# Kernel tuning notes

Hardware: AMD Instinct MI355X
Metric: run time of the kernel (lower is better)

The kernel has to match this reference:

```python
import jax, jax.numpy as jnp
import numpy as np

T, IN, OUT, R = 8192, 4096, 4096, 64


def setup_inputs() -> dict:
    key = jax.random.key(0)
    ks = jax.random.split(key, 7)
    # signed int4 values in [-8, 8) for activations and (unpacked) weights
    quant_x = jax.random.randint(ks[0], (T, IN), -8, 8, dtype=jnp.int32)
    weight_q = jax.random.randint(ks[1], (OUT, IN), -8, 8, dtype=jnp.int32)
    # positive per-token / per-channel symmetric-quant scales
    scale_x = jax.random.uniform(ks[2], (T,), dtype=jnp.float32) * 0.01 + 1e-4
    weight_scales = jax.random.uniform(ks[3], (OUT,), dtype=jnp.float32) * 0.01 + 1e-4
    outlier_x = jax.random.normal(ks[4], (T, R), dtype=jnp.float32)
    w_outlier = jax.random.normal(ks[5], (OUT, R), dtype=jnp.float32)
    bias = jax.random.normal(ks[6], (OUT,), dtype=jnp.float32)
    return {"quant_x": quant_x, "weight_q": weight_q, "scale_x": scale_x,
            "weight_scales": weight_scales, "outlier_x": outlier_x,
            "w_outlier": w_outlier, "bias": bias}


def reference(quant_x, weight_q, scale_x, weight_scales, outlier_x, w_outlier, bias):
    acc = jnp.matmul(quant_x, weight_q.T)
    # sym_dequant: per-row activation scale * per-column weight scale
    x_out = acc.astype(jnp.float32) * scale_x[:, None] * weight_scales[None, :]
    # outlier low-rank addmm + bias epilogue
    x_out = x_out + jnp.matmul(outlier_x, w_outlier.T) + bias
    return x_out
```

## Files before the change

kernel.cpp:

```cpp
#include <hip/hip_runtime.h>

#define T_DIM 8192
#define IN_DIM 4096
#define OUT_DIM 4096
#define R_DIM 64
#define NKP 32

typedef int i32x4 __attribute__((ext_vector_type(4)));
typedef float f32x4 __attribute__((ext_vector_type(4)));
typedef _Float16 f16x8 __attribute__((ext_vector_type(8)));

__device__ __forceinline__ int pack4(int4 v) {
  return (v.x & 255) | ((v.y & 255) << 8) | ((v.z & 255) << 16) | ((unsigned)v.w << 24);
}

__device__ __forceinline__ void gload16(const void* g, void* l) {
  __builtin_amdgcn_global_load_lds(
      (const __attribute__((address_space(1))) void*)(unsigned long long)g,
      (__attribute__((address_space(3))) void*)(unsigned)(unsigned long long)l,
      16, 0, 0);
}

__device__ __forceinline__ i32x4 unp(int x, int y) {
  i32x4 r;
  r[0] = x & 0x0F0F0F0F;
  r[1] = (x >> 4) & 0x0F0F0F0F;
  r[2] = y & 0x0F0F0F0F;
  r[3] = (y >> 4) & 0x0F0F0F0F;
  return r;
}

__device__ __forceinline__ unsigned pb(int a, int b) {
  return (unsigned)(a + 8) | ((unsigned)(b + 8) << 4);
}

__global__ __launch_bounds__(256)
void cvt_pack_kernel(const int* __restrict__ qx, const int* __restrict__ wq,
                     char* __restrict__ pk, int* __restrict__ SS) {
  const int wave = blockIdx.x * 4 + (threadIdx.x >> 6);
  const int l = threadIdx.x & 63;
  const int nw = gridDim.x * 4;
  for (int r = wave; r < T_DIM + OUT_DIM; r += nw) {
    const int* src = (r < T_DIM) ? (qx + (size_t)r * IN_DIM)
                                 : (wq + (size_t)(r - T_DIM) * IN_DIM);
    const int4* src4 = (const int4*)src;
    char* dst = pk + (size_t)r * 2048;
    const int rx = (r >> 1) & 3;
    int s = 0;
#pragma unroll
    for (int i = 0; i < 4; ++i) {
      const int q = i * 64 + l;
      const int kt = q >> 2, g = q & 3;
      int4 s0 = src4[q * 4 + 0], s1 = src4[q * 4 + 1];
      int4 s2 = src4[q * 4 + 2], s3 = src4[q * 4 + 3];
      s += s0.x + s0.y + s0.z + s0.w + s1.x + s1.y + s1.z + s1.w +
           s2.x + s2.y + s2.z + s2.w + s3.x + s3.y + s3.z + s3.w;
      unsigned dw0 = pb(s0.x, s0.y) | (pb(s0.z, s0.w) << 8) |
                     (pb(s1.x, s1.y) << 16) | (pb(s1.z, s1.w) << 24);
      unsigned dw1 = pb(s2.x, s2.y) | (pb(s2.z, s2.w) << 8) |
                     (pb(s3.x, s3.y) << 16) | (pb(s3.z, s3.w) << 24);
      const int off = (kt >> 1) * 64 + ((g ^ rx) << 4) + (kt & 1) * 8;
      *(uint2*)(dst + off) = make_uint2(dw0, dw1);
    }
#pragma unroll
    for (int off = 1; off < 64; off <<= 1) s += __shfl_xor(s, off, 64);
    if (l == 0) SS[r] = s + 8 * IN_DIM;
  }
}

__global__ __launch_bounds__(256)
void w4a4_gemm(const char* __restrict__ A8, const char* __restrict__ B8,
               const int* __restrict__ SS,
               const float* __restrict__ sx, const float* __restrict__ sw,
               const float* __restrict__ ox, const float* __restrict__ ow,
               const float* __restrict__ bias, float* __restrict__ out) {
  __shared__ __align__(16) char smem[49152];

  const int bid = blockIdx.x;
  const int swz = (bid & 7) * 256 + (bid >> 3);
  const int tm = swz >> 5, tn = swz & 31;
  const int brow = tm * 128, bcol = tn * 128;

  const int t = threadIdx.x;
  const int w = t >> 6, l = t & 63;
  const int wr = w >> 1, wc = w & 1;
  const int l16 = l & 15, lk = l >> 4;

  const char* gA0 = A8 + (size_t)(brow + (t >> 2)) * 2048 + (t & 3) * 16;
  const char* gA1 = gA0 + (size_t)64 * 2048;
  const char* gB0 = B8 + (size_t)(bcol + (t >> 2)) * 2048 + (t & 3) * 16;
  const char* gB1 = gB0 + (size_t)64 * 2048;
  char* const dA0 = smem + t * 16;
  char* const dA1 = smem + 4096 + t * 16;
  char* const dB0 = smem + 8192 + t * 16;
  char* const dB1 = smem + 12288 + t * 16;

  const int Ra = wr * 64 + l16;
  const int Cb = wc * 64 + l16;
  const char* aR = smem + Ra * 64 + ((lk ^ ((Ra >> 1) & 3)) << 4);
  const char* bR = smem + 8192 + Cb * 64 + ((lk ^ ((Cb >> 1) & 3)) << 4);

  i32x4 acc[4][4];
#pragma unroll
  for (int m = 0; m < 4; ++m)
#pragma unroll
    for (int n = 0; n < 4; ++n) acc[m][n] = (i32x4){0, 0, 0, 0};

  auto stage = [&](int kp) {
    const int off = kp << 6;
    const int buf = (kp % 3) * 16384;
    gload16(gA0 + off, dA0 + buf);
    gload16(gA1 + off, dA1 + buf);
    gload16(gB0 + off, dB0 + buf);
    gload16(gB1 + off, dB1 + buf);
  };

  auto compute = [&](int kp) {
    const int buf = (kp % 3) * 16384;
    const char* sa = aR + buf;
    const char* sb = bR + buf;
    i32x4 ap[4], bp[4];
#pragma unroll
    for (int m = 0; m < 4; ++m) ap[m] = *(const i32x4*)(sa + m * 1024);
#pragma unroll
    for (int n = 0; n < 4; ++n) bp[n] = *(const i32x4*)(sb + n * 1024);
    i32x4 bv[4];
#pragma unroll
    for (int n = 0; n < 4; ++n) bv[n] = unp(bp[n][0], bp[n][1]);
    __builtin_amdgcn_s_setprio(1);
#pragma unroll
    for (int m = 0; m < 4; ++m) {
      i32x4 av = unp(ap[m][0], ap[m][1]);
      acc[m][0] = __builtin_amdgcn_mfma_i32_16x16x64_i8(av, bv[0], acc[m][0], 0, 0, 0);
      acc[m][1] = __builtin_amdgcn_mfma_i32_16x16x64_i8(av, bv[1], acc[m][1], 0, 0, 0);
      acc[m][2] = __builtin_amdgcn_mfma_i32_16x16x64_i8(av, bv[2], acc[m][2], 0, 0, 0);
      acc[m][3] = __builtin_amdgcn_mfma_i32_16x16x64_i8(av, bv[3], acc[m][3], 0, 0, 0);
    }
    __builtin_amdgcn_s_setprio(0);
#pragma unroll
    for (int n = 0; n < 4; ++n) bv[n] = unp(bp[n][2], bp[n][3]);
    __builtin_amdgcn_s_setprio(1);
#pragma unroll
    for (int m = 0; m < 4; ++m) {
      i32x4 av = unp(ap[m][2], ap[m][3]);
      acc[m][0] = __builtin_amdgcn_mfma_i32_16x16x64_i8(av, bv[0], acc[m][0], 0, 0, 0);
      acc[m][1] = __builtin_amdgcn_mfma_i32_16x16x64_i8(av, bv[1], acc[m][1], 0, 0, 0);
      acc[m][2] = __builtin_amdgcn_mfma_i32_16x16x64_i8(av, bv[2], acc[m][2], 0, 0, 0);
      acc[m][3] = __builtin_amdgcn_mfma_i32_16x16x64_i8(av, bv[3], acc[m][3], 0, 0, 0);
    }
    __builtin_amdgcn_s_setprio(0);
  };

#define VMBAR(N)                                          \
  asm volatile("s_waitcnt vmcnt(" #N ")" ::: "memory");   \
  __builtin_amdgcn_s_barrier();                           \
  __builtin_amdgcn_sched_barrier(0);

  stage(0); stage(1);
  for (int kp = 0; kp < NKP - 2; ++kp) {
    VMBAR(4);
    stage(kp + 2);
    compute(kp);
  }
  VMBAR(4);
  compute(NKP - 2);
  VMBAR(0);
  compute(NKP - 1);

  const int orow0 = brow + wr * 64 + (lk << 2);
  const int ocol0 = bcol + wc * 64 + l16;
  const int* SA = SS;
  const int* SB = SS + T_DIM;
  float swv[4], bvv[4];
  int cb[4];
#pragma unroll
  for (int n = 0; n < 4; ++n) {
    swv[n] = sw[ocol0 + n * 16];
    bvv[n] = bias[ocol0 + n * 16];
    cb[n] = -8 * SB[ocol0 + n * 16];
  }

  f32x4 facc[4][4];
#pragma unroll
  for (int m = 0; m < 4; ++m) {
#pragma unroll
    for (int r = 0; r < 4; ++r) {
      const int row = orow0 + m * 16 + r;
      const float sxv = sx[row];
      const int ca = 262144 - 8 * SA[row];
#pragma unroll
      for (int n = 0; n < 4; ++n)
        facc[m][n][r] = (float)(acc[m][n][r] + ca + cb[n]) * sxv * swv[n];
    }
  }

  __syncthreads();
#pragma unroll
  for (int j = 0; j < 4; ++j) {
    int q = j * 256 + t;
    int row = q >> 3, cd = q & 7, cs = cd ^ (row & 7);
    const float* ga = ox + (size_t)(brow + row) * R_DIM + cs * 8;
    float4 f0 = *(const float4*)ga, f1 = *(const float4*)(ga + 4);
    f16x8 h;
    h[0] = (_Float16)f0.x; h[1] = (_Float16)f0.y; h[2] = (_Float16)f0.z; h[3] = (_Float16)f0.w;
    h[4] = (_Float16)f1.x; h[5] = (_Float16)f1.y; h[6] = (_Float16)f1.z; h[7] = (_Float16)f1.w;
    *(f16x8*)(smem + row * 128 + cd * 16) = h;
    const float* gb = ow + (size_t)(bcol + row) * R_DIM + cs * 8;
    f0 = *(const float4*)gb; f1 = *(const float4*)(gb + 4);
    f16x8 g;
    g[0] = (_Float16)f0.x; g[1] = (_Float16)f0.y; g[2] = (_Float16)f0.z; g[3] = (_Float16)f0.w;
    g[4] = (_Float16)f1.x; g[5] = (_Float16)f1.y; g[6] = (_Float16)f1.z; g[7] = (_Float16)f1.w;
    *(f16x8*)(smem + 16384 + row * 128 + cd * 16) = g;
  }
  __syncthreads();

  const char* qa = smem + (wr * 64 + l16) * 128;
  const char* qb = smem + 16384 + (wc * 64 + l16) * 128;
  const int x7 = l16 & 7;
#pragma unroll
  for (int s = 0; s < 2; ++s) {
    const int ca2 = ((s * 4 + lk) ^ x7) << 4;
    f16x8 hb[4];
#pragma unroll
    for (int n = 0; n < 4; ++n) hb[n] = *(const f16x8*)(qb + n * 2048 + ca2);
#pragma unroll
    for (int m = 0; m < 4; ++m) {
      f16x8 ha = *(const f16x8*)(qa + m * 2048 + ca2);
#pragma unroll
      for (int n = 0; n < 4; ++n)
        facc[m][n] = __builtin_amdgcn_mfma_f32_16x16x32_f16(ha, hb[n], facc[m][n], 0, 0, 0);
    }
  }

#pragma unroll
  for (int m = 0; m < 4; ++m)
#pragma unroll
    for (int r = 0; r < 4; ++r) {
      float* po = out + (size_t)(orow0 + m * 16 + r) * OUT_DIM + ocol0;
#pragma unroll
      for (int n = 0; n < 4; ++n) po[n * 16] = facc[m][n][r] + bvv[n];
    }
}

__global__ __launch_bounds__(256)
void w4a4_gemm_fb(const int* __restrict__ A32, const int* __restrict__ B32,
                  const float* __restrict__ sx, const float* __restrict__ sw,
                  const float* __restrict__ ox, const float* __restrict__ ow,
                  const float* __restrict__ bias, float* __restrict__ out) {
  __shared__ __align__(16) unsigned char smem[32768];
  char* sA = (char*)smem;
  char* sB = (char*)smem + 8192;

  const int bid = blockIdx.x;
  const int swzb = (bid & 7) * 256 + (bid >> 3);
  const int tm = swzb >> 5, tn = swzb & 31;
  const int brow = tm * 128, bcol = tn * 128;

  const int t = threadIdx.x;
  const int l = t & 63;
  const int wr = (t >> 6) >> 1, wc = (t >> 6) & 1;
  const int l16 = l & 15, lk = l >> 4;

  i32x4 iacc[4][4];
#pragma unroll
  for (int m = 0; m < 4; ++m)
#pragma unroll
    for (int n = 0; n < 4; ++n) iacc[m][n] = (i32x4){0, 0, 0, 0};

  const int ar = t >> 2;
  const int ac = (t & 3) << 4;
  const int* hA0 = A32 + (size_t)(brow + ar) * IN_DIM + ac;
  const int* hA1 = hA0 + (size_t)64 * IN_DIM;
  const int* hB0 = B32 + (size_t)(bcol + ar) * IN_DIM + ac;
  const int* hB1 = hB0 + (size_t)64 * IN_DIM;

  const char* fragA = sA + (size_t)(wr * 64 + l16) * 64 + lk * 16;
  const char* fragB = sB + (size_t)(wc * 64 + l16) * 64 + lk * 16;

  for (int k0 = 0; k0 < IN_DIM; k0 += 64) {
    const int4* pA0 = (const int4*)(hA0 + k0);
    int4 r0 = {pack4(pA0[0]), pack4(pA0[1]), pack4(pA0[2]), pack4(pA0[3])};
    *(int4*)(sA + t * 16) = r0;
    const int4* pA1 = (const int4*)(hA1 + k0);
    int4 r1 = {pack4(pA1[0]), pack4(pA1[1]), pack4(pA1[2]), pack4(pA1[3])};
    *(int4*)(sA + 4096 + t * 16) = r1;
    const int4* pB0 = (const int4*)(hB0 + k0);
    int4 r2 = {pack4(pB0[0]), pack4(pB0[1]), pack4(pB0[2]), pack4(pB0[3])};
    *(int4*)(sB + t * 16) = r2;
    const int4* pB1 = (const int4*)(hB1 + k0);
    int4 r3 = {pack4(pB1[0]), pack4(pB1[1]), pack4(pB1[2]), pack4(pB1[3])};
    *(int4*)(sB + 4096 + t * 16) = r3;
    __syncthreads();
    i32x4 av[4], bv[4];
#pragma unroll
    for (int m = 0; m < 4; ++m) av[m] = *(const i32x4*)(fragA + m * 1024);
#pragma unroll
    for (int n = 0; n < 4; ++n) bv[n] = *(const i32x4*)(fragB + n * 1024);
#pragma unroll
    for (int m = 0; m < 4; ++m)
#pragma unroll
      for (int n = 0; n < 4; ++n)
        iacc[m][n] = __builtin_amdgcn_mfma_i32_16x16x64_i8(av[m], bv[n], iacc[m][n], 0, 0, 0);
    __syncthreads();
  }

  const int orow = brow + wr * 64 + lk * 4;
  const int ocol = bcol + wc * 64 + l16;
  float swv[4], bvv[4];
#pragma unroll
  for (int n = 0; n < 4; ++n) { swv[n] = sw[ocol + n * 16]; bvv[n] = bias[ocol + n * 16]; }

  f32x4 facc[4][4];
#pragma unroll
  for (int m = 0; m < 4; ++m)
#pragma unroll
    for (int r = 0; r < 4; ++r) {
      float sxv = sx[orow + m * 16 + r];
#pragma unroll
      for (int n = 0; n < 4; ++n) facc[m][n][r] = (float)iacc[m][n][r] * sxv * swv[n];
    }

  _Float16* oA = (_Float16*)smem;
  _Float16* oB = (_Float16*)(smem + 16384);
#pragma unroll
  for (int j = 0; j < 4; ++j) {
    int c = j * 256 + t;
    int rr2 = c >> 3, c8 = (c & 7) << 3;
    const float* gp = ox + (size_t)(brow + rr2) * R_DIM + c8;
    float4 f0 = *(const float4*)gp;
    float4 f1 = *(const float4*)(gp + 4);
    f16x8 h;
    h[0] = (_Float16)f0.x; h[1] = (_Float16)f0.y; h[2] = (_Float16)f0.z; h[3] = (_Float16)f0.w;
    h[4] = (_Float16)f1.x; h[5] = (_Float16)f1.y; h[6] = (_Float16)f1.z; h[7] = (_Float16)f1.w;
    *(f16x8*)((char*)oA + (size_t)c * 16) = h;
    const float* gq = ow + (size_t)(bcol + rr2) * R_DIM + c8;
    f0 = *(const float4*)gq; f1 = *(const float4*)(gq + 4);
    f16x8 g;
    g[0] = (_Float16)f0.x; g[1] = (_Float16)f0.y; g[2] = (_Float16)f0.z; g[3] = (_Float16)f0.w;
    g[4] = (_Float16)f1.x; g[5] = (_Float16)f1.y; g[6] = (_Float16)f1.z; g[7] = (_Float16)f1.w;
    *(f16x8*)((char*)oB + (size_t)c * 16) = g;
  }
  __syncthreads();

  const char* qa = (const char*)oA + (size_t)(wr * 64 + l16) * 128 + lk * 16;
  const char* qb = (const char*)oB + (size_t)(wc * 64 + l16) * 128 + lk * 16;
#pragma unroll
  for (int s = 0; s < 2; ++s) {
    f16x8 ha[4], hb[4];
#pragma unroll
    for (int m = 0; m < 4; ++m) ha[m] = *(const f16x8*)(qa + m * 2048 + s * 64);
#pragma unroll
    for (int n = 0; n < 4; ++n) hb[n] = *(const f16x8*)(qb + n * 2048 + s * 64);
#pragma unroll
    for (int m = 0; m < 4; ++m)
#pragma unroll
      for (int n = 0; n < 4; ++n)
        facc[m][n] = __builtin_amdgcn_mfma_f32_16x16x32_f16(ha[m], hb[n], facc[m][n], 0, 0, 0);
  }

#pragma unroll
  for (int m = 0; m < 4; ++m)
#pragma unroll
    for (int r = 0; r < 4; ++r) {
      float* po = out + (size_t)(orow + m * 16 + r) * OUT_DIM + ocol;
#pragma unroll
      for (int n = 0; n < 4; ++n) po[n * 16] = facc[m][n][r] + bvv[n];
    }
}

extern "C" void kernel_launch(void* const* d_in, const int* in_sizes, int n_in,
                              void* d_out, int out_size, void* d_ws, size_t ws_size,
                              hipStream_t stream) {
  const int*   qx   = (const int*)d_in[0];
  const int*   wq   = (const int*)d_in[1];
  const float* sx   = (const float*)d_in[2];
  const float* sw   = (const float*)d_in[3];
  const float* ox   = (const float*)d_in[4];
  const float* ow   = (const float*)d_in[5];
  const float* bias = (const float*)d_in[6];
  float* out = (float*)d_out;

  const size_t packedA = (size_t)T_DIM * 2048;
  const size_t packedB = (size_t)OUT_DIM * 2048;
  const size_t ssBytes = (size_t)(T_DIM + OUT_DIM) * 4;
  const size_t need = packedA + packedB + ssBytes;

  if (ws_size >= need) {
    char* pk = (char*)d_ws;
    int* SS = (int*)(pk + packedA + packedB);
    cvt_pack_kernel<<<768, 256, 0, stream>>>(qx, wq, pk, SS);
    w4a4_gemm<<<2048, 256, 0, stream>>>(pk, pk + packedA, SS, sx, sw, ox, ow, bias, out);
  } else {
    w4a4_gemm_fb<<<2048, 256, 0, stream>>>(qx, wq, sx, sw, ox, ow, bias, out);
  }
}
```

Measured before the change: 183.9 us.

## Halve K-tile to 32 bytes, deepen pipeline to four stages, cut LDS for occupancy

The GEMM main loop now moves 32 bytes of packed K per row per stage (64 steps instead of 32) and uses a 4-deep ring of 8 KB buffers. Total shared memory drops from 48 KB to 32 KB, and launch bounds now request 4 blocks per CU. The packing kernel's layout and XOR swizzle are changed to match 8-byte reads. Block-to-tile mapping is redone per XCD so each XCD covers a contiguous region of tiles, aiming for better L2 reuse. The risk is twice as many barriers and waitcnts per tile with less MFMA work between them, plus register pressure from the occupancy target.

Measured after the change: 204.2 us. 11.0% more time.

```diff
diff --git a/kernel.cpp b/kernel.cpp
--- a/kernel.cpp
+++ b/kernel.cpp
@@ -4,7 +4,7 @@
 #define IN_DIM 4096
 #define OUT_DIM 4096
 #define R_DIM 64
-#define NKP 32
+#define NKT 64
 
 typedef int i32x4 __attribute__((ext_vector_type(4)));
 typedef float f32x4 __attribute__((ext_vector_type(4)));
@@ -45,21 +45,21 @@
                                  : (wq + (size_t)(r - T_DIM) * IN_DIM);
     const int4* src4 = (const int4*)src;
     char* dst = pk + (size_t)r * 2048;
-    const int rx = (r >> 1) & 3;
+    const int rq = (r >> 2) & 3;
     int s = 0;
 #pragma unroll
     for (int i = 0; i < 4; ++i) {
-      const int q = i * 64 + l;
-      const int kt = q >> 2, g = q & 3;
-      int4 s0 = src4[q * 4 + 0], s1 = src4[q * 4 + 1];
-      int4 s2 = src4[q * 4 + 2], s3 = src4[q * 4 + 3];
+      const int idx = i * 64 + l;
+      const int kt = idx >> 2, d = idx & 3;
+      int4 s0 = src4[idx * 4 + 0], s1 = src4[idx * 4 + 1];
+      int4 s2 = src4[idx * 4 + 2], s3 = src4[idx * 4 + 3];
       s += s0.x + s0.y + s0.z + s0.w + s1.x + s1.y + s1.z + s1.w +
            s2.x + s2.y + s2.z + s2.w + s3.x + s3.y + s3.z + s3.w;
       unsigned dw0 = pb(s0.x, s0.y) | (pb(s0.z, s0.w) << 8) |
                      (pb(s1.x, s1.y) << 16) | (pb(s1.z, s1.w) << 24);
       unsigned dw1 = pb(s2.x, s2.y) | (pb(s2.z, s2.w) << 8) |
                      (pb(s3.x, s3.y) << 16) | (pb(s3.z, s3.w) << 24);
-      const int off = (kt >> 1) * 64 + ((g ^ rx) << 4) + (kt & 1) * 8;
+      const int off = kt * 32 + ((d ^ rq) << 3);
       *(uint2*)(dst + off) = make_uint2(dw0, dw1);
     }
 #pragma unroll
@@ -68,37 +68,34 @@
   }
 }
 
-__global__ __launch_bounds__(256)
+__global__ __launch_bounds__(256, 4)
 void w4a4_gemm(const char* __restrict__ A8, const char* __restrict__ B8,
                const int* __restrict__ SS,
                const float* __restrict__ sx, const float* __restrict__ sw,
                const float* __restrict__ ox, const float* __restrict__ ow,
                const float* __restrict__ bias, float* __restrict__ out) {
-  __shared__ __align__(16) char smem[49152];
+  __shared__ __align__(16) char smem[32768];
 
   const int bid = blockIdx.x;
-  const int swz = (bid & 7) * 256 + (bid >> 3);
-  const int tm = swz >> 5, tn = swz & 31;
+  const int xcd = bid & 7, c = bid >> 3;
+  const int tn = (xcd & 3) * 8 + (c & 7);
+  const int tm = (xcd >> 2) * 32 + (c >> 3);
   const int brow = tm * 128, bcol = tn * 128;
 
   const int t = threadIdx.x;
   const int w = t >> 6, l = t & 63;
   const int wr = w >> 1, wc = w & 1;
   const int l16 = l & 15, lk = l >> 4;
-
-  const char* gA0 = A8 + (size_t)(brow + (t >> 2)) * 2048 + (t & 3) * 16;
-  const char* gA1 = gA0 + (size_t)64 * 2048;
-  const char* gB0 = B8 + (size_t)(bcol + (t >> 2)) * 2048 + (t & 3) * 16;
-  const char* gB1 = gB0 + (size_t)64 * 2048;
-  char* const dA0 = smem + t * 16;
-  char* const dA1 = smem + 4096 + t * 16;
-  char* const dB0 = smem + 8192 + t * 16;
-  char* const dB1 = smem + 12288 + t * 16;
-
-  const int Ra = wr * 64 + l16;
-  const int Cb = wc * 64 + l16;
-  const char* aR = smem + Ra * 64 + ((lk ^ ((Ra >> 1) & 3)) << 4);
-  const char* bR = smem + 8192 + Cb * 64 + ((lk ^ ((Cb >> 1) & 3)) << 4);
+  (void)w;
+
+  const char* gA = A8 + (size_t)(brow + (t >> 1)) * 2048 + (t & 1) * 16;
+  const char* gB = B8 + (size_t)(bcol + (t >> 1)) * 2048 + (t & 1) * 16;
+  char* const dA = smem + t * 16;
+  char* const dB = smem + 4096 + t * 16;
+
+  const int cho = (lk ^ ((l16 >> 2) & 3)) << 3;
+  const char* aR = smem + (wr * 64 + l16) * 32 + cho;
+  const char* bR = smem + 4096 + (wc * 64 + l16) * 32 + cho;
 
   i32x4 acc[4][4];
 #pragma unroll
@@ -106,47 +103,33 @@
 #pragma unroll
     for (int n = 0; n < 4; ++n) acc[m][n] = (i32x4){0, 0, 0, 0};
 
-  auto stage = [&](int kp) {
-    const int off = kp << 6;
-    const int buf = (kp % 3) * 16384;
-    gload16(gA0 + off, dA0 + buf);
-    gload16(gA1 + off, dA1 + buf);
-    gload16(gB0 + off, dB0 + buf);
-    gload16(gB1 + off, dB1 + buf);
+  auto stage = [&](int kt) {
+    const int off = kt << 5;
+    const int buf = (kt & 3) << 13;
+    gload16(gA + off, dA + buf);
+    gload16(gB + off, dB + buf);
   };
 
-  auto compute = [&](int kp) {
-    const int buf = (kp % 3) * 16384;
+  auto compute = [&](int kt) {
+    const int buf = (kt & 3) << 13;
     const char* sa = aR + buf;
     const char* sb = bR + buf;
-    i32x4 ap[4], bp[4];
-#pragma unroll
-    for (int m = 0; m < 4; ++m) ap[m] = *(const i32x4*)(sa + m * 1024);
-#pragma unroll
-    for (int n = 0; n < 4; ++n) bp[n] = *(const i32x4*)(sb + n * 1024);
-    i32x4 bv[4];
-#pragma unroll
-    for (int n = 0; n < 4; ++n) bv[n] = unp(bp[n][0], bp[n][1]);
+    int2 pa[4], pv[4];
+#pragma unroll
+    for (int m = 0; m < 4; ++m) pa[m] = *(const int2*)(sa + m * 512);
+#pragma unroll
+    for (int n = 0; n < 4; ++n) pv[n] = *(const int2*)(sb + n * 512);
+    i32x4 bu[4];
+#pragma unroll
+    for (int n = 0; n < 4; ++n) bu[n] = unp(pv[n].x, pv[n].y);
     __builtin_amdgcn_s_setprio(1);
 #pragma unroll
     for (int m = 0; m < 4; ++m) {
-      i32x4 av = unp(ap[m][0], ap[m][1]);
-      acc[m][0] = __builtin_amdgcn_mfma_i32_16x16x64_i8(av, bv[0], acc[m][0], 0, 0, 0);
-      acc[m][1] = __builtin_amdgcn_mfma_i32_16x16x64_i8(av, bv[1], acc[m][1], 0, 0, 0);
-      acc[m][2] = __builtin_amdgcn_mfma_i32_16x16x64_i8(av, bv[2], acc[m][2], 0, 0, 0);
-      acc[m][3] = __builtin_amdgcn_mfma_i32_16x16x64_i8(av, bv[3], acc[m][3], 0, 0, 0);
-    }
-    __builtin_amdgcn_s_setprio(0);
-#pragma unroll
-    for (int n = 0; n < 4; ++n) bv[n] = unp(bp[n][2], bp[n][3]);
-    __builtin_amdgcn_s_setprio(1);
-#pragma unroll
-    for (int m = 0; m < 4; ++m) {
-      i32x4 av = unp(ap[m][2], ap[m][3]);
-      acc[m][0] = __builtin_amdgcn_mfma_i32_16x16x64_i8(av, bv[0], acc[m][0], 0, 0, 0);
-      acc[m][1] = __builtin_amdgcn_mfma_i32_16x16x64_i8(av, bv[1], acc[m][1], 0, 0, 0);
-      acc[m][2] = __builtin_amdgcn_mfma_i32_16x16x64_i8(av, bv[2], acc[m][2], 0, 0, 0);
-      acc[m][3] = __builtin_amdgcn_mfma_i32_16x16x64_i8(av, bv[3], acc[m][3], 0, 0, 0);
+      i32x4 au = unp(pa[m].x, pa[m].y);
+      acc[m][0] = __builtin_amdgcn_mfma_i32_16x16x64_i8(au, bu[0], acc[m][0], 0, 0, 0);
+      acc[m][1] = __builtin_amdgcn_mfma_i32_16x16x64_i8(au, bu[1], acc[m][1], 0, 0, 0);
+      acc[m][2] = __builtin_amdgcn_mfma_i32_16x16x64_i8(au, bu[2], acc[m][2], 0, 0, 0);
+      acc[m][3] = __builtin_amdgcn_mfma_i32_16x16x64_i8(au, bu[3], acc[m][3], 0, 0, 0);
     }
     __builtin_amdgcn_s_setprio(0);
   };
@@ -156,16 +139,18 @@
   __builtin_amdgcn_s_barrier();                           \
   __builtin_amdgcn_sched_barrier(0);
 
-  stage(0); stage(1);
-  for (int kp = 0; kp < NKP - 2; ++kp) {
+  stage(0); stage(1); stage(2);
+  for (int kt = 0; kt < NKT - 3; ++kt) {
     VMBAR(4);
-    stage(kp + 2);
-    compute(kp);
+    stage(kt + 3);
+    compute(kt);
   }
   VMBAR(4);
-  compute(NKP - 2);
+  compute(NKT - 3);
+  VMBAR(2);
+  compute(NKT - 2);
   VMBAR(0);
-  compute(NKP - 1);
+  compute(NKT - 1);
 
   const int orow0 = brow + wr * 64 + (lk << 2);
   const int ocol0 = bcol + wc * 64 + l16;
```
